# Kernel optimization log

Hardware: AMD Instinct MI355X
Metric: run time of the kernel (lower is better)

## Reference

```python
import jax, jax.numpy as jnp
import numpy as np

ALPHA = 0.2  # LeakyReLU slope
BN_EPS = 1e-5


def _conv_circ(x, w, b, pad_w):
    # circular padding only on width (torch padding=(0, pad_w), padding_mode='circular')
    x = jnp.pad(x, ((0, 0), (0, 0), (0, 0), (pad_w, pad_w)), mode='wrap')
    y = jax.lax.conv_general_dilated(x, w, window_strides=(1, 1), padding='VALID',
                                     dimension_numbers=('NCHW', 'OIHW', 'NCHW'))
    return y + b[None, :, None, None]


def _graph_conv(x, n, w, b, pad_w):
    h1 = _conv_circ(x, w, b, pad_w)  # [B, N, C, F]
    h2 = _conv_circ(n, w, b, pad_w)
    B, N, C, F = h1.shape
    h1f = h1.reshape(B, N, C * F)
    h2f = h2.reshape(B, N, C * F)
    a = jnp.einsum('bnf,bmf->bnm', h1f, h2f)          # [B, N, N]
    a = jnp.where(a > 0, a, ALPHA * a)                 # LeakyReLU
    att = jax.nn.softmax(a, axis=1)                    # torch Softmax(dim=1)
    return (att @ h1f).reshape(B, N, C, F)


def _bn_pool_relu(x, gamma, beta, mean, var):
    # eval-mode BatchNorm2d -> MaxPool2d((1,2)) -> ReLU
    inv = gamma / jnp.sqrt(var + BN_EPS)
    x = x * inv[None, :, None, None] + (beta - mean * inv)[None, :, None, None]
    W = x.shape[-1]
    W2 = (W // 2) * 2
    x = x[..., :W2].reshape(*x.shape[:-1], W2 // 2, 2).max(axis=-1)
    return jax.nn.relu(x)


def setup_inputs() -> dict:
    key = jax.random.key(0)
    ks = jax.random.split(key, 16)
    B = 16384
    return {
        'x': jax.random.normal(ks[0], (B, 5, 5, 50), jnp.float32),
        'conv1_w': jax.random.normal(ks[1], (32, 5, 5, 11), jnp.float32) * 0.1,
        'conv1_b': jax.random.normal(ks[2], (32,), jnp.float32) * 0.1,
        'bn1_gamma': jax.random.uniform(ks[3], (32,), jnp.float32, 0.5, 1.5),
        'bn1_beta': jax.random.normal(ks[4], (32,), jnp.float32) * 0.1,
        'bn1_mean': jax.random.normal(ks[5], (32,), jnp.float32) * 0.1,
        'bn1_var': jax.random.uniform(ks[6], (32,), jnp.float32, 0.5, 1.5),
        'conv2_w': jax.random.normal(ks[7], (32, 32, 1, 5), jnp.float32) * 0.1,
        'conv2_b': jax.random.normal(ks[8], (32,), jnp.float32) * 0.1,
        'bn2_gamma': jax.random.uniform(ks[9], (32,), jnp.float32, 0.5, 1.5),
        'bn2_beta': jax.random.normal(ks[10], (32,), jnp.float32) * 0.1,
        'bn2_mean': jax.random.normal(ks[11], (32,), jnp.float32) * 0.1,
        'bn2_var': jax.random.uniform(ks[12], (32,), jnp.float32, 0.5, 1.5),
        'lin_w': jax.random.normal(ks[13], (13, 384), jnp.float32) * 0.05,
        'lin_b': jax.random.normal(ks[14], (13,), jnp.float32) * 0.05,
    }


def reference(x, conv1_w, conv1_b, bn1_gamma, bn1_beta, bn1_mean, bn1_var,
              conv2_w, conv2_b, bn2_gamma, bn2_beta, bn2_mean, bn2_var,
              lin_w, lin_b):
    W = x.shape[-1]
    xa, na = x[..., :W // 2], x[..., W // 2:]
    xa = _graph_conv(xa, xa, conv1_w, conv1_b, 5)
    na = _graph_conv(na, na, conv1_w, conv1_b, 5)
    xa = _bn_pool_relu(xa, bn1_gamma, bn1_beta, bn1_mean, bn1_var)
    na = _bn_pool_relu(na, bn1_gamma, bn1_beta, bn1_mean, bn1_var)
    x2 = _graph_conv(xa, na, conv2_w, conv2_b, 2)
    n2 = _graph_conv(na, xa, conv2_w, conv2_b, 2)
    x2 = _bn_pool_relu(x2, bn2_gamma, bn2_beta, bn2_mean, bn2_var)
    n2 = _bn_pool_relu(n2, bn2_gamma, bn2_beta, bn2_mean, bn2_var)
    flat = jnp.concatenate([x2, n2], axis=-1).reshape(x.shape[0], -1)  # [B, 384]
    # Dropout(0.2) is identity in eval mode
    return flat @ lin_w.T + lin_b
```

## Files before the change

kernel.cpp:

```cpp
#include <hip/hip_runtime.h>
#include <math.h>

#define ALPHA 0.2f
#define BN_EPS 1e-5f

typedef __attribute__((ext_vector_type(8))) short short8;
typedef __attribute__((ext_vector_type(4))) float v4f;

__device__ __forceinline__ unsigned short f2bf_rne(float f) {
    union { float f; unsigned u; } x; x.f = f;
    unsigned r = x.u + 0x7FFFu + ((x.u >> 16) & 1u);
    return (unsigned short)(r >> 16);
}
__device__ __forceinline__ float bf2f(unsigned short h) {
    union { float f; unsigned u; } x; x.u = ((unsigned)h) << 16;
    return x.f;
}
__device__ __forceinline__ unsigned cvtpk_bf16(float a0, float a1) {
    unsigned r;
    asm("v_cvt_pk_bf16_f32 %0, %1, %2" : "=v"(r) : "v"(a0), "v"(a1));
    return r;
}
__device__ __forceinline__ void hilo_pair(float a0, float a1, unsigned& hp, unsigned& lp) {
    hp = cvtpk_bf16(a0, a1);
    union { unsigned u; float f; } c0, c1;
    c0.u = hp << 16; c1.u = hp & 0xFFFF0000u;
    lp = cvtpk_bf16(a0 - c0.f, a1 - c1.f);
}
__device__ __forceinline__ unsigned funnel16(unsigned hi, unsigned lo, int sh) {
    return (unsigned)((((unsigned long long)hi << 32) | lo) >> sh);
}

__global__ __launch_bounds__(256) void prep_kernel(const float* __restrict__ w1,
                                                   const float* __restrict__ w2,
                                                   unsigned short* __restrict__ ws16) {
    int s = blockIdx.x * 256 + threadIdx.x;
    if (s < 1664) {
        int lane = s & 63;
        int ktnt = s >> 6;
        int Kt = ktnt % 13;
        int Nt = ktnt / 13;
        int oc = Nt * 16 + (lane & 15);
        int quad = lane >> 4;
        for (int j = 0; j < 8; ++j) {
            int kp = Kt * 32 + quad * 8 + j;
            int kw = kp & 15, ickh = kp >> 4;
            float w = 0.f;
            if (kw < 11 && ickh < 25) w = w1[oc * 275 + ickh * 11 + kw];
            unsigned short h = f2bf_rne(w);
            ws16[s * 8 + j] = h;
            ws16[13312 + s * 8 + j] = f2bf_rne(w - bf2f(h));
        }
    } else if (s < 2304) {
        int s2 = s - 1664;
        int lane = s2 & 63;
        int ktnt = s2 >> 6;
        int kw = ktnt >> 1;
        int nt = ktnt & 1;
        int oc = nt * 16 + (lane & 15);
        int quad = lane >> 4;
        for (int j = 0; j < 8; ++j) {
            int ic = quad * 8 + j;
            float w = w2[oc * 160 + ic * 5 + kw];
            unsigned short h = f2bf_rne(w);
            ws16[26624 + s2 * 8 + j] = h;
            ws16[31744 + s2 * 8 + j] = f2bf_rne(w - bf2f(h));
        }
    }
}

#define IT 3848
#define XBO 1716
#define ATO 1716
#define CSTO 7696
#define LDS_TOTAL (7696 + 128)

__global__ __launch_bounds__(256, 5) void gcn_kernel(
    const float* __restrict__ x,
    const float* __restrict__ w1, const float* __restrict__ b1,
    const float* __restrict__ g1, const float* __restrict__ be1,
    const float* __restrict__ mu1, const float* __restrict__ va1,
    const float* __restrict__ w2, const float* __restrict__ b2,
    const float* __restrict__ g2, const float* __restrict__ be2,
    const float* __restrict__ mu2, const float* __restrict__ va2,
    const float* __restrict__ lw, const float* __restrict__ lb,
    const unsigned short* __restrict__ ws16,
    float* __restrict__ out)
{
    __shared__ float lds[LDS_TOTAL];
    float* cst = lds + CSTO;

    const int tid = threadIdx.x;
    const int b0  = blockIdx.x * 2;

    {
        const float2* xg2 = (const float2*)(x + (size_t)b0 * 1250);
        for (int i2 = tid; i2 < 1250; i2 += 256) {
            float2 v = xg2[i2];
            int i = 2 * i2;
            int it = (i >= 1250) ? 1 : 0;
            int j = i - it * 1250;
            unsigned short* XU = (unsigned short*)(lds + it * IT + XBO);
            {
                int c = j / 250; int r = j - c * 250;
                int h = r / 50;  int w50 = r - h * 50;
                int ha = (w50 >= 25) ? 1 : 0;
                int w = w50 - ha * 25;
                int base = (ha * 25 + c * 5 + h) * 42;
                unsigned short u = f2bf_rne(v.x);
                XU[base + 5 + w] = u;
                if (w >= 20) XU[base + w - 20] = u;
                if (w <= 9)  XU[base + 30 + w] = u;
            }
            {
                int j1 = j + 1;
                int c = j1 / 250; int r = j1 - c * 250;
                int h = r / 50;  int w51 = r - h * 50;
                int hb = (w51 >= 25) ? 1 : 0;
                int w = w51 - hb * 25;
                int base = (hb * 25 + c * 5 + h) * 42;
                unsigned short u = f2bf_rne(v.y);
                XU[base + 5 + w] = u;
                if (w >= 20) XU[base + w - 20] = u;
                if (w <= 9)  XU[base + 30 + w] = u;
            }
        }
        if (tid < 42) {
            int itz = (tid >= 21) ? 1 : 0;
            lds[itz * IT + XBO + 1050 + (tid - itz * 21)] = 0.f;
        }
    }
    if (tid < 64) {
        int oc = tid & 31;
        if (tid < 32) {
            float inv = g1[oc] * rsqrtf(va1[oc] + BN_EPS);
            cst[oc]      = inv;
            cst[32 + oc] = be1[oc] - mu1[oc] * inv;
        } else {
            float inv = g2[oc] * rsqrtf(va2[oc] + BN_EPS);
            cst[64 + oc] = inv;
            cst[96 + oc] = be2[oc] - mu2[oc] * inv;
        }
    }
    __syncthreads();

    {
        const int wave = tid >> 6, lane = tid & 63;
        const int it = wave >> 1;
        const int Mtb = (wave & 1) * 2;
        const int quad = lane >> 4, m16 = lane & 15;
        const int kw0 = (quad & 1) * 8;
        const int ickh0 = quad >> 1;
        const unsigned* XD = (const unsigned*)(lds + it * IT + XBO);

        int ub[2], sh[2];
#pragma unroll
        for (int mt = 0; mt < 2; ++mt) {
            int mg = (Mtb + mt) * 16 + m16;
            int half = (mg >= 25) ? 1 : 0;
            int pos = mg - half * 25; pos = (pos > 24) ? 24 : pos;
            int ux = (half * 25 + ickh0) * 42 + pos + kw0;
            ub[mt] = ux >> 1;
            sh[mt] = (ux & 1) << 4;
        }

        v4f zz = {0.f, 0.f, 0.f, 0.f};
        v4f acc[2][2];
        acc[0][0] = zz; acc[0][1] = zz; acc[1][0] = zz; acc[1][1] = zz;

        for (int Kt = 0; Kt < 13; ++Kt) {
            union { unsigned u[4]; short8 v; } af[2];
#pragma unroll
            for (int mt = 0; mt < 2; ++mt) {
                int b = ub[mt] + Kt * 42;
                unsigned d0 = XD[b + 0], d1 = XD[b + 1], d2 = XD[b + 2];
                unsigned d3 = XD[b + 3], d4 = XD[b + 4];
                af[mt].u[0] = funnel16(d1, d0, sh[mt]);
                af[mt].u[1] = funnel16(d2, d1, sh[mt]);
                af[mt].u[2] = funnel16(d3, d2, sh[mt]);
                af[mt].u[3] = funnel16(d4, d3, sh[mt]);
            }
#pragma unroll
            for (int nt = 0; nt < 2; ++nt) {
                const short8* ph = (const short8*)(ws16 + ((nt * 13 + Kt) * 64 + lane) * 8);
                const short8* pl = (const short8*)(ws16 + 13312 + ((nt * 13 + Kt) * 64 + lane) * 8);
                short8 bh = *ph;
                short8 bl = *pl;
#pragma unroll
                for (int mt = 0; mt < 2; ++mt) {
                    acc[mt][nt] = __builtin_amdgcn_mfma_f32_16x16x32_bf16(af[mt].v, bh, acc[mt][nt], 0, 0, 0);
                    acc[mt][nt] = __builtin_amdgcn_mfma_f32_16x16x32_bf16(af[mt].v, bl, acc[mt][nt], 0, 0, 0);
                }
            }
        }

        float bias0 = b1[m16], bias1 = b1[16 + m16];
        unsigned short* U = (unsigned short*)(lds + it * IT);
#pragma unroll
        for (int mt = 0; mt < 2; ++mt) {
#pragma unroll
            for (int r = 0; r < 4; ++r) {
                int mg = (Mtb + mt) * 16 + quad * 4 + r;
                if (mg < 50) {
                    int half = (mg >= 25) ? 1 : 0;
                    int pos = mg - half * 25;
                    int kd = pos >> 1, par = pos & 1;
                    float v0 = acc[mt][0][r] + bias0;
                    float v1 = acc[mt][1][r] + bias1;
                    int ch0 = half * 32 + m16;
                    int ch1 = half * 32 + 16 + m16;
                    unsigned short h0 = f2bf_rne(v0);
                    unsigned short h1v = f2bf_rne(v1);
                    U[kd * 132 + ch0 * 2 + par] = h0;
                    U[1716 + kd * 132 + ch0 * 2 + par] = f2bf_rne(v0 - bf2f(h0));
                    U[kd * 132 + ch1 * 2 + par] = h1v;
                    U[1716 + kd * 132 + ch1 * 2 + par] = f2bf_rne(v1 - bf2f(h1v));
                }
            }
        }
    }
    __syncthreads();

    {
        const int wave = tid >> 6, lane = tid & 63;
        const int it = wave >> 1, half = wave & 1;
        const int m16 = lane & 15, q = lane >> 4;
        const unsigned* D = (const unsigned*)(lds + it * IT);
        short8 fh[2], fl[2];
#pragma unroll
        for (int t = 0; t < 2; ++t) {
            int row = half * 32 + t * 16 + m16;
            union { unsigned u[4]; short8 v; } H, L;
#pragma unroll
            for (int i = 0; i < 4; ++i) {
                int k0 = q * 8 + 2 * i;
                unsigned mh = D[(k0 >> 1) * 66 + row];
                unsigned ml = D[858 + (k0 >> 1) * 66 + row];
                if (k0 == 24) { mh &= 0xFFFFu; ml &= 0xFFFFu; }
                if (k0 > 24)  { mh = 0u; ml = 0u; }
                H.u[i] = mh; L.u[i] = ml;
            }
            fh[t] = H.v; fl[t] = L.v;
        }
        v4f zz = {0.f, 0.f, 0.f, 0.f};
        v4f acc[2][2];
        acc[0][0] = zz; acc[0][1] = zz; acc[1][0] = zz; acc[1][1] = zz;
#pragma unroll
        for (int mt = 0; mt < 2; ++mt)
#pragma unroll
            for (int nt = 0; nt < 2; ++nt) {
                acc[mt][nt] = __builtin_amdgcn_mfma_f32_16x16x32_bf16(fh[mt], fh[nt], acc[mt][nt], 0, 0, 0);
                acc[mt][nt] = __builtin_amdgcn_mfma_f32_16x16x32_bf16(fh[mt], fl[nt], acc[mt][nt], 0, 0, 0);
                acc[mt][nt] = __builtin_amdgcn_mfma_f32_16x16x32_bf16(fl[mt], fh[nt], acc[mt][nt], 0, 0, 0);
            }
        float* A = &lds[it * IT + ATO];
#pragma unroll
        for (int mt = 0; mt < 2; ++mt)
#pragma unroll
            for (int nt = 0; nt < 2; ++nt)
#pragma unroll
                for (int r = 0; r < 4; ++r) {
                    int m = mt * 16 + q * 4 + r;
                    int n = nt * 16 + m16;
                    float s = acc[mt][nt][r];
                    s = (s > 0.f) ? s : ALPHA * s;
                    A[(half * 32 + m) * 33 + n] = s;
                }
    }
    __syncthreads();

    {
        int row = tid >> 1, q = tid & 1;
        int it = row >> 6, rm = row & 63;
        float* rp = &lds[it * IT + ATO + rm * 33];
        float ev[16];
        float mx = -INFINITY;
#pragma unroll
        for (int k = 0; k < 16; ++k) { ev[k] = rp[q + 2 * k]; mx = fmaxf(mx, ev[k]); }
        mx = fmaxf(mx, __shfl_xor(mx, 1));
        float s = 0.f;
#pragma unroll
        for (int k = 0; k < 16; ++k) { ev[k] = __expf(ev[k] - mx); s += ev[k]; }
        s += __shfl_xor(s, 1);
        float inv = 1.f / s;
#pragma unroll
        for (int k = 0; k < 16; ++k) rp[q + 2 * k] = ev[k] * inv;
    }
    __syncthreads();

    {
        const int wave = tid >> 6, lane = tid & 63;
        const int it = wave >> 1, half = wave & 1;
        const int m16 = lane & 15, q = lane >> 4;
        const unsigned short* U = (const unsigned short*)(lds + it * IT);
        const float* AT = &lds[it * IT + ATO];

        short8 ah[2], al[2];
#pragma unroll
        for (int mt = 0; mt < 2; ++mt) {
            int pos = mt * 16 + m16;
            int kd = pos >> 1, par = pos & 1;
            union { unsigned u[4]; short8 v; } H, L;
#pragma unroll
            for (int i = 0; i < 4; ++i) {
                int ch = half * 32 + q * 8 + 2 * i;
                unsigned h0 = U[kd * 132 + ch * 2 + par];
                unsigned h1u = U[kd * 132 + (ch + 1) * 2 + par];
                unsigned l0 = U[1716 + kd * 132 + ch * 2 + par];
                unsigned l1 = U[1716 + kd * 132 + (ch + 1) * 2 + par];
                H.u[i] = h0 | (h1u << 16);
                L.u[i] = l0 | (l1 << 16);
            }
            ah[mt] = H.v; al[mt] = L.v;
        }
        short8 bh[2], bl[2];
#pragma unroll
        for (int nt = 0; nt < 2; ++nt) {
            union { unsigned u[4]; short8 v; } H, L;
#pragma unroll
            for (int i = 0; i < 4; ++i) {
                int m = q * 8 + 2 * i;
                float a0 = AT[(half * 32 + m) * 33 + nt * 16 + m16];
                float a1 = AT[(half * 32 + m + 1) * 33 + nt * 16 + m16];
                unsigned hp, lp;
                hilo_pair(a0, a1, hp, lp);
                H.u[i] = hp; L.u[i] = lp;
            }
            bh[nt] = H.v; bl[nt] = L.v;
        }
        v4f zz = {0.f, 0.f, 0.f, 0.f};
        v4f acc[2][2];
        acc[0][0] = zz; acc[0][1] = zz; acc[1][0] = zz; acc[1][1] = zz;
#pragma unroll
        for (int mt = 0; mt < 2; ++mt)
#pragma unroll
            for (int nt = 0; nt < 2; ++nt) {
                acc[mt][nt] = __builtin_amdgcn_mfma_f32_16x16x32_bf16(ah[mt], bh[nt], acc[mt][nt], 0, 0, 0);
                acc[mt][nt] = __builtin_amdgcn_mfma_f32_16x16x32_bf16(ah[mt], bl[nt], acc[mt][nt], 0, 0, 0);
                acc[mt][nt] = __builtin_amdgcn_mfma_f32_16x16x32_bf16(al[mt], bh[nt], acc[mt][nt], 0, 0, 0);
            }

        __syncthreads();

        unsigned short* PT = (unsigned short*)(lds + it * IT) + half * 832;
#pragma unroll
        for (int mt = 0; mt < 2; ++mt)
#pragma unroll
            for (int nt = 0; nt < 2; ++nt) {
                int n = nt * 16 + m16;
                float inv = cst[n], sh = cst[32 + n];
#pragma unroll
                for (int rr = 0; rr < 2; ++rr) {
                    int pos0 = mt * 16 + q * 4 + rr * 2;
                    if (pos0 < 24) {
                        float v0 = acc[mt][nt][rr * 2] * inv + sh;
                        float v1 = acc[mt][nt][rr * 2 + 1] * inv + sh;
                        float p = fmaxf(fmaxf(v0, v1), 0.f);
                        int j = pos0 >> 1;
                        unsigned short h = f2bf_rne(p);
                        PT[(n >> 1) * 26 + j * 2 + (n & 1)] = h;
                        PT[416 + (n >> 1) * 26 + j * 2 + (n & 1)] = f2bf_rne(p - bf2f(h));
                    }
                }
            }
    }
    __syncthreads();

    {
        const int wave = tid >> 6, lane = tid & 63;
        const int it = wave >> 1, half = wave & 1;
        const int m16 = lane & 15, q = lane >> 4;
        const unsigned* PTD = (const unsigned*)(lds + it * IT) + half * 416;

        v4f zz = {0.f, 0.f, 0.f, 0.f};
        v4f acc[2]; acc[0] = zz; acc[1] = zz;
#pragma unroll
        for (int kw = 0; kw < 5; ++kw) {
            int owr = m16 + kw - 2;
            if (owr < 0) owr += 12;
            if (owr >= 12) owr -= 12;
            union { unsigned u[4]; short8 v; } H, L;
#pragma unroll
            for (int i = 0; i < 4; ++i) {
                H.u[i] = PTD[(q * 4 + i) * 13 + owr];
                L.u[i] = PTD[208 + (q * 4 + i) * 13 + owr];
            }
#pragma unroll
            for (int nt = 0; nt < 2; ++nt) {
                const short8* ph = (const short8*)(ws16 + 26624 + ((kw * 2 + nt) * 64 + lane) * 8);
                const short8* pl = (const short8*)(ws16 + 31744 + ((kw * 2 + nt) * 64 + lane) * 8);
                short8 wbh = *ph, wbl = *pl;
                acc[nt] = __builtin_amdgcn_mfma_f32_16x16x32_bf16(H.v, wbh, acc[nt], 0, 0, 0);
                acc[nt] = __builtin_amdgcn_mfma_f32_16x16x32_bf16(H.v, wbl, acc[nt], 0, 0, 0);
                acc[nt] = __builtin_amdgcn_mfma_f32_16x16x32_bf16(L.v, wbh, acc[nt], 0, 0, 0);
            }
        }
        if (q < 3) {
            unsigned* H2 = (unsigned*)(lds + it * IT) + 858;
#pragma unroll
            for (int nt = 0; nt < 2; ++nt) {
                float bias = b2[nt * 16 + m16];
                int ch = half * 32 + nt * 16 + m16;
#pragma unroll
                for (int rr = 0; rr < 2; ++rr) {
                    float v0 = acc[nt][rr * 2] + bias;
                    float v1 = acc[nt][rr * 2 + 1] + bias;
                    unsigned hp, lp;
                    hilo_pair(v0, v1, hp, lp);
                    H2[(q * 2 + rr) * 66 + ch] = hp;
                    H2[396 + (q * 2 + rr) * 66 + ch] = lp;
                }
            }
        }
    }
    __syncthreads();

    {
        const int wave = tid >> 6, lane = tid & 63;
        const int it = wave >> 1, half = wave & 1;
        const int m16 = lane & 15, q = lane >> 4;
        const unsigned* D = (const unsigned*)(lds + it * IT) + 858;
        short8 ah[2], al[2], bh[2], bl[2];
#pragma unroll
        for (int t = 0; t < 2; ++t) {
            int rowA = (1 - half) * 32 + t * 16 + m16;
            int rowB = half * 32 + t * 16 + m16;
            union { unsigned u[4]; short8 v; } HA, LA, HB, LB;
#pragma unroll
            for (int i = 0; i < 4; ++i) {
                int k0 = q * 8 + 2 * i;
                unsigned a_h = D[(k0 >> 1) * 66 + rowA];
                unsigned a_l = D[396 + (k0 >> 1) * 66 + rowA];
                unsigned b_h = D[(k0 >> 1) * 66 + rowB];
                unsigned b_l = D[396 + (k0 >> 1) * 66 + rowB];
                if (k0 > 10) { a_h = 0u; a_l = 0u; b_h = 0u; b_l = 0u; }
                HA.u[i] = a_h; LA.u[i] = a_l; HB.u[i] = b_h; LB.u[i] = b_l;
            }
            ah[t] = HA.v; al[t] = LA.v; bh[t] = HB.v; bl[t] = LB.v;
        }
        v4f zz = {0.f, 0.f, 0.f, 0.f};
        v4f acc[2][2];
        acc[0][0] = zz; acc[0][1] = zz; acc[1][0] = zz; acc[1][1] = zz;
#pragma unroll
        for (int mt = 0; mt < 2; ++mt)
#pragma unroll
            for (int nt = 0; nt < 2; ++nt) {
                acc[mt][nt] = __builtin_amdgcn_mfma_f32_16x16x32_bf16(ah[mt], bh[nt], acc[mt][nt], 0, 0, 0);
                acc[mt][nt] = __builtin_amdgcn_mfma_f32_16x16x32_bf16(ah[mt], bl[nt], acc[mt][nt], 0, 0, 0);
                acc[mt][nt] = __builtin_amdgcn_mfma_f32_16x16x32_bf16(al[mt], bh[nt], acc[mt][nt], 0, 0, 0);
            }
        float* A = &lds[it * IT + ATO];
#pragma unroll
        for (int mt = 0; mt < 2; ++mt)
#pragma unroll
            for (int nt = 0; nt < 2; ++nt)
#pragma unroll
                for (int r = 0; r < 4; ++r) {
                    int m = mt * 16 + q * 4 + r;
                    int n = nt * 16 + m16;
                    float s = acc[mt][nt][r];
                    s = (s > 0.f) ? s : ALPHA * s;
                    A[(half * 32 + m) * 33 + n] = s;
                }
    }
    __syncthreads();

    {
        int row = tid >> 1, q = tid & 1;
        int it = row >> 6, rm = row & 63;
        float* rp = &lds[it * IT + ATO + rm * 33];
        float ev[16];
        float mx = -INFINITY;
#pragma unroll
        for (int k = 0; k < 16; ++k) { ev[k] = rp[q + 2 * k]; mx = fmaxf(mx, ev[k]); }
        mx = fmaxf(mx, __shfl_xor(mx, 1));
        float s = 0.f;
#pragma unroll
        for (int k = 0; k < 16; ++k) { ev[k] = __expf(ev[k] - mx); s += ev[k]; }
        s += __shfl_xor(s, 1);
        float inv = 1.f / s;
#pragma unroll
        for (int k = 0; k < 16; ++k) rp[q + 2 * k] = ev[k] * inv;
    }
    __syncthreads();

    {
        const int wave = tid >> 6, lane = tid & 63;
        const int it = wave >> 1, half = wave & 1;
        const int m16 = lane & 15, q = lane >> 4;
        const unsigned short* U = (const unsigned short*)(lds + it * IT);
        const float* AT = &lds[it * IT + ATO];

        int kd = m16 >> 1, par = m16 & 1;
        union { unsigned u[4]; short8 v; } HA, LA;
#pragma unroll
        for (int i = 0; i < 4; ++i) {
            int ch = half * 32 + q * 8 + 2 * i;
            unsigned h0 = U[1716 + kd * 132 + ch * 2 + par];
            unsigned h1u = U[1716 + kd * 132 + (ch + 1) * 2 + par];
            unsigned l0 = U[2508 + kd * 132 + ch * 2 + par];
            unsigned l1 = U[2508 + kd * 132 + (ch + 1) * 2 + par];
            HA.u[i] = h0 | (h1u << 16);
            LA.u[i] = l0 | (l1 << 16);
        }
        short8 bh[2], bl[2];
#pragma unroll
        for (int nt = 0; nt < 2; ++nt) {
            union { unsigned u[4]; short8 v; } H, L;
#pragma unroll
            for (int i = 0; i < 4; ++i) {
                int m = q * 8 + 2 * i;
                float a0 = AT[(half * 32 + m) * 33 + nt * 16 + m16];
                float a1 = AT[(half * 32 + m + 1) * 33 + nt * 16 + m16];
                unsigned hp, lp;
                hilo_pair(a0, a1, hp, lp);
                H.u[i] = hp; L.u[i] = lp;
            }
            bh[nt] = H.v; bl[nt] = L.v;
        }
        v4f zz = {0.f, 0.f, 0.f, 0.f};
        v4f acc[2]; acc[0] = zz; acc[1] = zz;
#pragma unroll
        for (int nt = 0; nt < 2; ++nt) {
            acc[nt] = __builtin_amdgcn_mfma_f32_16x16x32_bf16(HA.v, bh[nt], acc[nt], 0, 0, 0);
            acc[nt] = __builtin_amdgcn_mfma_f32_16x16x32_bf16(HA.v, bl[nt], acc[nt], 0, 0, 0);
            acc[nt] = __builtin_amdgcn_mfma_f32_16x16x32_bf16(LA.v, bh[nt], acc[nt], 0, 0, 0);
        }
        if (q < 3) {
#pragma unroll
            for (int nt = 0; nt < 2; ++nt) {
                int n = nt * 16 + m16;
                float inv = cst[64 + n], sh = cst[96 + n];
#pragma unroll
                for (int rr = 0; rr < 2; ++rr) {
                    int j = q * 2 + rr;
                    float v0 = acc[nt][rr * 2] * inv + sh;
                    float v1 = acc[nt][rr * 2 + 1] * inv + sh;
                    lds[it * IT + n * 12 + half * 6 + j] =
                        fmaxf(fmaxf(v0, v1), 0.f);
                }
            }
        }
    }
    __syncthreads();

    if (tid < 208) {
        int s8 = tid & 7;
        int rest = tid >> 3;
        int it = (rest >= 13) ? 1 : 0;
        int o = rest - it * 13;
        const float4* wv4 = (const float4*)(lw + o * 384 + s8 * 48);
        const float4* fv4 = (const float4*)&lds[it * IT + s8 * 48];
        float s = 0.f;
#pragma unroll
        for (int i = 0; i < 12; ++i) {
            float4 w4 = wv4[i];
            float4 f4 = fv4[i];
            s += f4.x * w4.x + f4.y * w4.y + f4.z * w4.z + f4.w * w4.w;
        }
        s += __shfl_down(s, 4, 8);
        s += __shfl_down(s, 2, 8);
        s += __shfl_down(s, 1, 8);
        if (s8 == 0) out[(size_t)(b0 + it) * 13 + o] = s + lb[o];
    }
}

extern "C" void kernel_launch(void* const* d_in, const int* in_sizes, int n_in,
                              void* d_out, int out_size, void* d_ws, size_t ws_size,
                              hipStream_t stream) {
    const float* x   = (const float*)d_in[0];
    const float* w1  = (const float*)d_in[1];
    const float* b1  = (const float*)d_in[2];
    const float* g1  = (const float*)d_in[3];
    const float* be1 = (const float*)d_in[4];
    const float* mu1 = (const float*)d_in[5];
    const float* va1 = (const float*)d_in[6];
    const float* w2  = (const float*)d_in[7];
    const float* b2  = (const float*)d_in[8];
    const float* g2  = (const float*)d_in[9];
    const float* be2 = (const float*)d_in[10];
    const float* mu2 = (const float*)d_in[11];
    const float* va2 = (const float*)d_in[12];
    const float* lw  = (const float*)d_in[13];
    const float* lb  = (const float*)d_in[14];
    float* out = (float*)d_out;
    unsigned short* ws16 = (unsigned short*)d_ws;

    prep_kernel<<<9, 256, 0, stream>>>(w1, w2, ws16);

    int B = in_sizes[0] / 1250;
    gcn_kernel<<<B / 2, 256, 0, stream>>>(x, w1, b1, g1, be1, mu1, va1,
                                          w2, b2, g2, be2, mu2, va2, lw, lb,
                                          ws16, out);
}
```

Measured before the change: 290.3 us.

## Shrink per-item LDS footprint to raise occupancy and drop a lo-part MFMA

Repacks the per-item LDS layout (smaller IT stride, aliased attention and hi/lo buffers) so the block uses less shared memory, and raises launch bounds from 5 to 6 blocks per CU. Extra __syncthreads are added where regions are now reused. The stage-1 output is stored as packed hi/lo pairs, and the first attention@h product drops the lo×hi MFMA term, reducing precision slightly. Added barriers and register pressure at the higher occupancy target may offset the gains.

```diff
diff --git a/kernel.cpp b/kernel.cpp
--- a/kernel.cpp
+++ b/kernel.cpp
@@ -69,13 +69,13 @@
     }
 }
 
-#define IT 3848
-#define XBO 1716
-#define ATO 1716
-#define CSTO 7696
-#define LDS_TOTAL (7696 + 128)
-
-__global__ __launch_bounds__(256, 5) void gcn_kernel(
+#define IT 2984
+#define HLO 858
+#define XB 1716
+#define CSTO 5968
+#define LDS_TOTAL (5968 + 128)
+
+__global__ __launch_bounds__(256, 6) void gcn_kernel(
     const float* __restrict__ x,
     const float* __restrict__ w1, const float* __restrict__ b1,
     const float* __restrict__ g1, const float* __restrict__ be1,
@@ -100,7 +100,7 @@
             int i = 2 * i2;
             int it = (i >= 1250) ? 1 : 0;
             int j = i - it * 1250;
-            unsigned short* XU = (unsigned short*)(lds + it * IT + XBO);
+            unsigned short* XU = (unsigned short*)(lds + it * IT + XB);
             {
                 int c = j / 250; int r = j - c * 250;
                 int h = r / 50;  int w50 = r - h * 50;
@@ -127,7 +127,7 @@
         }
         if (tid < 42) {
             int itz = (tid >= 21) ? 1 : 0;
-            lds[itz * IT + XBO + 1050 + (tid - itz * 21)] = 0.f;
+            lds[itz * IT + XB + 1050 + (tid - itz * 21)] = 0.f;
         }
     }
     if (tid < 64) {
@@ -151,14 +151,13 @@
         const int quad = lane >> 4, m16 = lane & 15;
         const int kw0 = (quad & 1) * 8;
         const int ickh0 = quad >> 1;
-        const unsigned* XD = (const unsigned*)(lds + it * IT + XBO);
+        const unsigned* XD = (const unsigned*)(lds + it * IT + XB);
 
         int ub[2], sh[2];
 #pragma unroll
         for (int mt = 0; mt < 2; ++mt) {
             int mg = (Mtb + mt) * 16 + m16;
-            int half = (mg >= 25) ? 1 : 0;
-            int pos = mg - half * 25; pos = (pos > 24) ? 24 : pos;
+            int half = mg >> 5, pos = mg & 31;
             int ux = (half * 25 + ickh0) * 42 + pos + kw0;
             ub[mt] = ux >> 1;
             sh[mt] = (ux & 1) << 4;
@@ -194,27 +193,27 @@
             }
         }
 
-        float bias0 = b1[m16], bias1 = b1[16 + m16];
-        unsigned short* U = (unsigned short*)(lds + it * IT);
+        float biasv0 = b1[m16], biasv1 = b1[16 + m16];
+        unsigned* HD = (unsigned*)(lds + it * IT);
 #pragma unroll
         for (int mt = 0; mt < 2; ++mt) {
 #pragma unroll
-            for (int r = 0; r < 4; ++r) {
-                int mg = (Mtb + mt) * 16 + quad * 4 + r;
-                if (mg < 50) {
-                    int half = (mg >= 25) ? 1 : 0;
-                    int pos = mg - half * 25;
-                    int kd = pos >> 1, par = pos & 1;
-                    float v0 = acc[mt][0][r] + bias0;
-                    float v1 = acc[mt][1][r] + bias1;
-                    int ch0 = half * 32 + m16;
-                    int ch1 = half * 32 + 16 + m16;
-                    unsigned short h0 = f2bf_rne(v0);
-                    unsigned short h1v = f2bf_rne(v1);
-                    U[kd * 132 + ch0 * 2 + par] = h0;
-                    U[1716 + kd * 132 + ch0 * 2 + par] = f2bf_rne(v0 - bf2f(h0));
-                    U[kd * 132 + ch1 * 2 + par] = h1v;
-                    U[1716 + kd * 132 + ch1 * 2 + par] = f2bf_rne(v1 - bf2f(h1v));
+            for (int rr = 0; rr < 2; ++rr) {
+                int mg0 = (Mtb + mt) * 16 + quad * 4 + rr * 2;
+                int half = mg0 >> 5, pos0 = mg0 & 31;
+                if (pos0 <= 24) {
+                    int kd = pos0 >> 1;
+#pragma unroll
+                    for (int nt = 0; nt < 2; ++nt) {
+                        float bias = nt ? biasv1 : biasv0;
+                        float v0 = acc[mt][nt][rr * 2] + bias;
+                        float v1 = acc[mt][nt][rr * 2 + 1] + bias;
+                        unsigned hp, lp;
+                        hilo_pair(v0, v1, hp, lp);
+                        int ch = half * 32 + nt * 16 + m16;
+                        HD[kd * 66 + ch] = hp;
+                        HD[858 + kd * 66 + ch] = lp;
+                    }
                 }
             }
         }
@@ -253,7 +252,8 @@
                 acc[mt][nt] = __builtin_amdgcn_mfma_f32_16x16x32_bf16(fh[mt], fl[nt], acc[mt][nt], 0, 0, 0);
                 acc[mt][nt] = __builtin_amdgcn_mfma_f32_16x16x32_bf16(fl[mt], fh[nt], acc[mt][nt], 0, 0, 0);
             }
-        float* A = &lds[it * IT + ATO];
+        __syncthreads();
+        float* A = &lds[it * IT + HLO];
 #pragma unroll
         for (int mt = 0; mt < 2; ++mt)
 #pragma unroll
@@ -272,7 +272,7 @@
     {
         int row = tid >> 1, q = tid & 1;
         int it = row >> 6, rm = row & 63;
-        float* rp = &lds[it * IT + ATO + rm * 33];
+        float* rp = &lds[it * IT + HLO + rm * 33];
         float ev[16];
         float mx = -INFINITY;
 #pragma unroll
@@ -293,25 +293,22 @@
         const int it = wave >> 1, half = wave & 1;
         const int m16 = lane & 15, q = lane >> 4;
         const unsigned short* U = (const unsigned short*)(lds + it * IT);
-        const float* AT = &lds[it * IT + ATO];
-
-        short8 ah[2], al[2];
+        const float* AT = &lds[it * IT + HLO];
+
+        short8 ah[2];
 #pragma unroll
         for (int mt = 0; mt < 2; ++mt) {
             int pos = mt * 16 + m16;
             int kd = pos >> 1, par = pos & 1;
-            union { unsigned u[4]; short8 v; } H, L;
+            union { unsigned u[4]; short8 v; } H;
 #pragma unroll
             for (int i = 0; i < 4; ++i) {
                 int ch = half * 32 + q * 8 + 2 * i;
                 unsigned h0 = U[kd * 132 + ch * 2 + par];
                 unsigned h1u = U[kd * 132 + (ch + 1) * 2 + par];
-                unsigned l0 = U[1716 + kd * 132 + ch * 2 + par];
-                unsigned l1 = U[1716 + kd * 132 + (ch + 1) * 2 + par];
                 H.u[i] = h0 | (h1u << 16);
-                L.u[i] = l0 | (l1 << 16);
-            }
-            ah[mt] = H.v; al[mt] = L.v;
+            }
+            ah[mt] = H.v;
         }
         short8 bh[2], bl[2];
 #pragma unroll
@@ -337,7 +334,6 @@
             for (int nt = 0; nt < 2; ++nt) {
                 acc[mt][nt] = __builtin_amdgcn_mfma_f32_16x16x32_bf16(ah[mt], bh[nt], acc[mt][nt], 0, 0, 0);
                 acc[mt][nt] = __builtin_amdgcn_mfma_f32_16x16x32_bf16(ah[mt], bl[nt], acc[mt][nt], 0, 0, 0);
-                acc[mt][nt] = __builtin_amdgcn_mfma_f32_16x16x32_bf16(al[mt], bh[nt], acc[mt][nt], 0, 0, 0);
             }
 
         __syncthreads();
@@ -395,8 +391,11 @@
                 acc[nt] = __builtin_amdgcn_mfma_f32_16x16x32_bf16(L.v, wbh, acc[nt], 0, 0, 0);
             }
         }
+
+        __syncthreads();
+
         if (q < 3) {
-            unsigned* H2 = (unsigned*)(lds + it * IT) + 858;
+            unsigned* H2 = (unsigned*)(lds + it * IT);
 #pragma unroll
             for (int nt = 0; nt < 2; ++nt) {
                 float bias = b2[nt * 16 + m16];
@@ -419,7 +418,7 @@
         const int wave = tid >> 6, lane = tid & 63;
         const int it = wave >> 1, half = wave & 1;
         const int m16 = lane & 15, q = lane >> 4;
-        const unsigned* D = (const unsigned*)(lds + it * IT) + 858;
+        const unsigned* D = (const unsigned*)(lds + it * IT);
         short8 ah[2], al[2], bh[2], bl[2];
 #pragma unroll
         for (int t = 0; t < 2; ++t) {
@@ -449,7 +448,7 @@
                 acc[mt][nt] = __builtin_amdgcn_mfma_f32_16x16x32_bf16(ah[mt], bl[nt], acc[mt][nt], 0, 0, 0);
                 acc[mt][nt] = __builtin_amdgcn_mfma_f32_16x16x32_bf16(al[mt], bh[nt], acc[mt][nt], 0, 0, 0);
             }
-        float* A = &lds[it * IT + ATO];
+        float* A = &lds[it * IT + HLO];
 #pragma unroll
         for (int mt = 0; mt < 2; ++mt)
 #pragma unroll
@@ -468,7 +467,7 @@
     {
         int row = tid >> 1, q = tid & 1;
         int it = row >> 6, rm = row & 63;
-        float* rp = &lds[it * IT + ATO + rm * 33];
+        float* rp = &lds[it * IT + HLO + rm * 33];
         float ev[16];
         float mx = -INFINITY;
 #pragma unroll
@@ -489,17 +488,17 @@
         const int it = wave >> 1, half = wave & 1;
         const int m16 = lane & 15, q = lane >> 4;
         const unsigned short* U = (const unsigned short*)(lds + it * IT);
-        const float* AT = &lds[it * IT + ATO];
+        const float* AT = &lds[it * IT + HLO];
 
         int kd = m16 >> 1, par = m16 & 1;
         union { unsigned u[4]; short8 v; } HA, LA;
 #pragma unroll
         for (int i = 0; i < 4; ++i) {
             int ch = half * 32 + q * 8 + 2 * i;
-            unsigned h0 = U[1716 + kd * 132 + ch * 2 + par];
-            unsigned h1u = U[1716 + kd * 132 + (ch + 1) * 2 + par];
-            unsigned l0 = U[2508 + kd * 132 + ch * 2 + par];
-            unsigned l1 = U[2508 + kd * 132 + (ch + 1) * 2 + par];
+            unsigned h0 = U[kd * 132 + ch * 2 + par];
+            unsigned h1u = U[kd * 132 + (ch + 1) * 2 + par];
+            unsigned l0 = U[792 + kd * 132 + ch * 2 + par];
+            unsigned l1 = U[792 + kd * 132 + (ch + 1) * 2 + par];
             HA.u[i] = h0 | (h1u << 16);
             LA.u[i] = l0 | (l1 << 16);
         }
@@ -526,6 +525,9 @@
             acc[nt] = __builtin_amdgcn_mfma_f32_16x16x32_bf16(HA.v, bl[nt], acc[nt], 0, 0, 0);
             acc[nt] = __builtin_amdgcn_mfma_f32_16x16x32_bf16(LA.v, bh[nt], acc[nt], 0, 0, 0);
         }
+
+        __syncthreads();
+
         if (q < 3) {
 #pragma unroll
             for (int nt = 0; nt < 2; ++nt) {
```

Result: faster. 271.9 us (-6.3%).
